# Kernel optimization log

Measured on AMD Instinct MI355X. Metric: run time of the kernel, lower is better.

## Reference

```python
import jax, jax.numpy as jnp
import numpy as np

B = 8
T_SCALES = 2
SEQ_LEN = 720
PRED_LEN = 720
ENC_IN = 862
MARK = 4
D_MODEL = 256
N_HEADS = 8
D_FF = 512
D_BLOCK = 720  # == PRED_LEN -> align is Identity
E_LAYERS = 2
EPS = 1e-5


def _ln(x, g, b):
    m = x.mean(-1, keepdims=True)
    v = ((x - m) ** 2).mean(-1, keepdims=True)
    return (x - m) / jnp.sqrt(v + EPS) * g + b


def setup_inputs() -> dict:
    key = jax.random.key(0)
    ks = iter(jax.random.split(key, 64))
    def rn(shape, s=0.02):
        return jax.random.normal(next(ks), shape, jnp.float32) * s
    L, d = E_LAYERS, D_MODEL
    inp = {}
    inp["multi_batch_x"] = jax.random.normal(next(ks), (B, T_SCALES, SEQ_LEN, ENC_IN), jnp.float32)
    inp["multi_batch_x_mark"] = jax.random.normal(next(ks), (B, T_SCALES, SEQ_LEN, MARK), jnp.float32)
    inp["x_dec"] = jnp.zeros((1,), jnp.float32)
    inp["x_mark_dec"] = jnp.zeros((1,), jnp.float32)
    inp["embed_w"] = rn((d, SEQ_LEN)); inp["embed_b"] = jnp.zeros((d,), jnp.float32)
    for nm in ("Wq", "Wk", "Wv", "Wo", "W3", "W4"):
        inp[nm] = rn((L, d, d))
    for nm in ("bq", "bk", "bv", "bo", "b3", "b4"):
        inp[nm] = jnp.zeros((L, d), jnp.float32)
    inp["W1"] = rn((L, D_FF, d)); inp["b1"] = jnp.zeros((L, D_FF), jnp.float32)
    inp["W2"] = rn((L, d, D_FF)); inp["b2"] = jnp.zeros((L, d), jnp.float32)
    inp["W5"] = rn((L, D_BLOCK, 2 * d)); inp["b5"] = jnp.zeros((L, D_BLOCK), jnp.float32)
    inp["W6"] = rn((L, D_BLOCK, 2 * d)); inp["b6"] = jnp.zeros((L, D_BLOCK), jnp.float32)
    inp["ln1_g"] = jnp.ones((L, d), jnp.float32); inp["ln1_b"] = jnp.zeros((L, d), jnp.float32)
    inp["ln2_g"] = jnp.ones((L, d), jnp.float32); inp["ln2_b"] = jnp.zeros((L, d), jnp.float32)
    return inp


def reference(multi_batch_x, multi_batch_x_mark, x_dec, x_mark_dec,
              embed_w, embed_b, Wq, bq, Wk, bk, Wv, bv, Wo, bo,
              W1, b1, W2, b2, W3, b3, W4, b4, W5, b5, W6, b6,
              ln1_g, ln1_b, ln2_g, ln2_b):
    H = N_HEADS
    E = D_MODEL // H
    Bc = multi_batch_x.shape[0]
    scale = 1.0 / jnp.sqrt(jnp.asarray(E, jnp.float32))
    outs = []
    for t in range(T_SCALES):
        x = multi_batch_x[:, t].transpose(0, 2, 1)            # [B, ENC_IN, S]
        mean = x.mean(-1, keepdims=True)
        std = jnp.sqrt(((x - mean) ** 2).mean(-1, keepdims=True) + EPS)
        xn = (x - mean) / std
        xm = multi_batch_x_mark[:, t].transpose(0, 2, 1)      # [B, MARK, S]
        xin = jnp.concatenate([xn, xm], axis=1)               # [B, N, S], N = ENC_IN+MARK
        h = jnp.einsum('bns,ds->bnd', xin, embed_w) + embed_b  # [B, N, d_model]
        N = xin.shape[1]
        output = jnp.zeros((Bc, N, D_BLOCK), h.dtype)
        for l in range(E_LAYERS):
            # full attention (mask_flag=False), dropout in eval mode = identity
            q = (h @ Wq[l].T + bq[l]).reshape(Bc, N, H, E)
            k = (h @ Wk[l].T + bk[l]).reshape(Bc, N, H, E)
            v = (h @ Wv[l].T + bv[l]).reshape(Bc, N, H, E)
            scores = jnp.einsum('blhe,bshe->bhls', q, k) * scale
            A = jax.nn.softmax(scores, axis=-1)
            att = jnp.einsum('bhls,bshd->blhd', A, v).reshape(Bc, N, H * E)
            x_att = att @ Wo[l].T + bo[l]
            x_ln = _ln(h - x_att, ln1_g[l], ln1_b[l])
            # 1x1 conv FFN (conv over channel dim == linear over feature dim)
            y = jax.nn.gelu(x_ln @ W1[l].T + b1[l], approximate=False) @ W2[l].T + b2[l]
            xs = x_ln - y                                      # subtract-residual
            hh = jax.nn.sigmoid(xs @ W3[l].T + b3[l]) * (xs @ W4[l].T + b4[l])
            cat = jnp.concatenate([x_att, y], axis=-1)         # [B, N, 2*d_model]
            out = jax.nn.sigmoid(cat @ W5[l].T + b5[l]) * (cat @ W6[l].T + b6[l])
            h = _ln(hh, ln2_g[l], ln2_b[l])
            output = out - output
        # align = Identity (D_BLOCK == PRED_LEN); keep first ENC_IN channels, invert scaler
        dec = output[:, :ENC_IN, :] * std + mean               # [B, ENC_IN, PRED_LEN]
        outs.append(dec.transpose(0, 2, 1))                    # [B, PRED_LEN, ENC_IN]
    return jnp.stack(outs, axis=-1).mean(axis=-1)
```

## Files before the change

### kernel.cpp

```cpp
#include <hip/hip_runtime.h>
#include <cstdint>
#include <cstddef>

#define DEV __device__ __forceinline__
#define AS1 __attribute__((address_space(1)))
#define AS3 __attribute__((address_space(3)))

typedef unsigned short u16;
typedef unsigned char u8;
typedef long long ll;

typedef __attribute__((ext_vector_type(8))) __bf16 bf16x8;
typedef __attribute__((ext_vector_type(8))) unsigned short u16x8;
typedef __attribute__((ext_vector_type(4))) float f32x4;

static constexpr int SEQ  = 720;
static constexpr int ENC  = 862;
static constexpr int NTOK = 866;
static constexpr int DM   = 256;
static constexpr int G16  = 16;
static constexpr int MTOT = G16 * NTOK;
static constexpr int KPAD = 768;
static constexpr int SPAD = 896;
static constexpr int TCH  = 15;
static constexpr float SC2 = 0.17677669529663689f * 1.4426950408889634f;

DEV float b2f(u16 v){ union { unsigned u; float f; } x; x.u = ((unsigned)v) << 16; return x.f; }
DEV u16 f2b(float f){ union { float f; unsigned u; } x; x.f = f;
  unsigned r = x.u + 0x7fffu + ((x.u >> 16) & 1u); return (u16)(r >> 16); }
DEV bf16x8 as_bf(u16x8 v){ return __builtin_bit_cast(bf16x8, v); }

DEV void g2l(const u16* g, u16* l){
  __builtin_amdgcn_global_load_lds((AS1 void*)g, (AS3 void*)l, 16, 0, 0);
}

DEV int xcd_work(){
  int L = blockIdx.y * gridDim.x + blockIdx.x;
  int T = gridDim.x * gridDim.y;
  int x = L & 7, k = L >> 3;
  int q = T >> 3, r = T & 7;
  int mn = x < r ? x : r;
  return x*q + mn + k;
}

struct CvtJobs {
  const float* src[10];
  u16* dst[10];
  int n[10];
  int per[10];
  ll stride[10];
};
__global__ __launch_bounds__(256) void cvt_multi(CvtJobs J)
{
  int j = blockIdx.y;
  const float* s = J.src[j];
  u16* d = J.dst[j];
  int n = J.n[j], per = J.per[j];
  ll st = J.stride[j];
  for (int i = blockIdx.x*256 + threadIdx.x; i < n; i += gridDim.x*256) {
    ll di = per ? ((ll)(i/per)*st + (i%per)) : (ll)i;
    d[di] = f2b(s[i]);
  }
}

__global__ __launch_bounds__(256) void pack_bqkv(const float* __restrict__ bq,
                                                 const float* __restrict__ bk,
                                                 const float* __restrict__ bv,
                                                 float* __restrict__ out)
{
  int idx = blockIdx.x*256 + threadIdx.x;
  if (idx >= 1536) return;
  int l = idx / 768, j = idx % 768;
  float v;
  if (j < 256)      v = bq[l*256 + j];
  else if (j < 512) v = bk[l*256 + j - 256];
  else              v = bv[l*256 + j - 512];
  out[idx] = v;
}

__global__ __launch_bounds__(256) void stats_part(const float* __restrict__ x,
                                                  float2* __restrict__ part)
{
  int g  = blockIdx.z;
  int tc = blockIdx.y;
  int c  = (blockIdx.x << 8) + threadIdx.x;
  float s = 0.f, q = 0.f;
  if (c < ENC) {
    const float* xp = x + ((ll)g * SEQ + tc * 48) * ENC + c;
    #pragma unroll 8
    for (int t = 0; t < 48; ++t) {
      float v = xp[(ll)t * ENC];
      s += v; q += v * v;
    }
  }
  part[(((ll)g * TCH + tc) * 4 + blockIdx.x) * 256 + threadIdx.x] = make_float2(s, q);
}

__global__ __launch_bounds__(256) void stats_reduce(const float2* __restrict__ part,
                                                    float* __restrict__ meanp,
                                                    float* __restrict__ stdp)
{
  int g  = blockIdx.x >> 2;
  int cc = blockIdx.x & 3;
  int c  = (cc << 8) + threadIdx.x;
  if (c >= ENC) return;
  float s = 0.f, q = 0.f;
  #pragma unroll
  for (int t = 0; t < TCH; ++t) {
    float2 p = part[(((ll)g * TCH + t) * 4 + cc) * 256 + threadIdx.x];
    s += p.x; q += p.y;
  }
  float mn  = s * (1.f / SEQ);
  float var = q * (1.f / SEQ) - mn * mn;
  var = var < 0.f ? 0.f : var;
  meanp[g * ENC + c] = mn;
  stdp [g * ENC + c] = sqrtf(var + 1e-5f);
}

__global__ __launch_bounds__(256) void build_xin(const float* __restrict__ x,
                                                 const float* __restrict__ xm,
                                                 const float* __restrict__ meanp,
                                                 const float* __restrict__ stdp,
                                                 u16* __restrict__ xin)
{
  int g  = blockIdx.z;
  int c0 = blockIdx.x << 5, s0 = blockIdx.y << 5;
  __shared__ float tl[32][33];
  __shared__ float mn[32], isd[32];
  int tid = threadIdx.x;
  if (tid < 32) {
    int c = c0 + tid;
    float m = 0.f, s = 1.f;
    if (c < ENC) { m = meanp[g*ENC + c]; s = stdp[g*ENC + c]; }
    mn[tid] = m; isd[tid] = 1.f / s;
  }
  __syncthreads();
  int ci = tid & 31, r = tid >> 5;
  #pragma unroll
  for (int p = 0; p < 4; ++p) {
    int sl = r + (p << 3);
    int s = s0 + sl, c = c0 + ci;
    float v = 0.f;
    if (s < SEQ && c < NTOK) {
      if (c < ENC) v = (x[((ll)g*SEQ + s)*ENC + c] - mn[ci]) * isd[ci];
      else         v = xm[((ll)g*SEQ + s)*4 + (c - ENC)];
    }
    tl[sl][ci] = v;
  }
  __syncthreads();
  int si = tid & 31;
  #pragma unroll
  for (int p = 0; p < 4; ++p) {
    int cl = r + (p << 3);
    int c = c0 + cl;
    if (c < NTOK) xin[((ll)g*NTOK + c)*KPAD + s0 + si] = f2b(tl[si][cl]);
  }
}

__global__ __launch_bounds__(256) void pack_embedw(const float* __restrict__ ew,
                                                   u16* __restrict__ wp)
{
  int row = blockIdx.x;
  for (int c = threadIdx.x; c < KPAD; c += 256)
    wp[row*KPAD + c] = (c < SEQ) ? f2b(ew[row*SEQ + c]) : (u16)0;
}

__global__ __launch_bounds__(256) void transpose_v(const u16* __restrict__ v, int ldv,
                                                   u16* __restrict__ vT)
{
  int g = blockIdx.z;
  int d0 = blockIdx.x << 5, s0 = blockIdx.y << 5;
  __shared__ u16 tl[32][33];
  int tid = threadIdx.x;
  int di = tid & 31, r = tid >> 5;
  #pragma unroll
  for (int p = 0; p < 4; ++p) {
    int sl = r + (p << 3);
    int s = s0 + sl;
    u16 val = 0;
    if (s < NTOK) val = v[((ll)g*NTOK + s)*ldv + d0 + di];
    tl[sl][di] = val;
  }
  __syncthreads();
  int si = tid & 31;
  #pragma unroll
  for (int p = 0; p < 4; ++p) {
    int dl = r + (p << 3);
    vT[((ll)g*DM + d0 + dl)*SPAD + s0 + si] = tl[si][dl];
  }
}

__global__ __launch_bounds__(256) void flash_attn(const u16* __restrict__ qb,
                                                  const u16* __restrict__ kb,
                                                  int ldqk,
                                                  const u16* __restrict__ vT,
                                                  u16* __restrict__ attb)
{
  const int w = xcd_work();
  const int gh = w / 7;
  const int g = gh >> 3, h = gh & 7;
  const int q0 = (w % 7) * 128;
  const int tid = threadIdx.x, wv = tid >> 6, lane = tid & 63;
  const int q4 = lane >> 4, c16 = lane & 15;
  constexpr int PLD = 136;

  __shared__ __attribute__((aligned(16))) u16 Qs[128*32];
  __shared__ __attribute__((aligned(16))) u16 Ks[128*32];
  __shared__ __attribute__((aligned(16))) u16 Vs[32*PLD];
  __shared__ __attribute__((aligned(16))) u16 Ps[4][32*PLD];

  {
    int r = tid >> 1, sg = (tid & 1) << 4;
    int row = q0 + r; if (row > NTOK-1) row = NTOK-1;
    const u16* src = qb + ((ll)(g*NTOK + row))*ldqk + h*32 + sg;
    *(uint4*)&Qs[r*32 + sg]     = *(const uint4*)src;
    *(uint4*)&Qs[r*32 + sg + 8] = *(const uint4*)(src + 8);
  }
  __syncthreads();

  bf16x8 qf[2];
  qf[0] = as_bf(*(const u16x8*)&Qs[(wv*32 +      c16)*32 + q4*8]);
  qf[1] = as_bf(*(const u16x8*)&Qs[(wv*32 + 16 + c16)*32 + q4*8]);

  float lsum[2][4] = {{0,0,0,0},{0,0,0,0}};
  f32x4 oacc[2][2];
  oacc[0][0] = (f32x4){0,0,0,0}; oacc[0][1] = (f32x4){0,0,0,0};
  oacc[1][0] = (f32x4){0,0,0,0}; oacc[1][1] = (f32x4){0,0,0,0};

  for (int kt = 0; kt < 7; ++kt) {
    const int k0 = kt * 128;
    if (kt) __syncthreads();
    {
      int r = tid >> 1, sg = (tid & 1) << 4;
      int row = k0 + r; if (row > NTOK-1) row = NTOK-1;
      const u16* src = kb + ((ll)(g*NTOK + row))*ldqk + h*32 + sg;
      *(uint4*)&Ks[r*32 + sg]     = *(const uint4*)src;
      *(uint4*)&Ks[r*32 + sg + 8] = *(const uint4*)(src + 8);
    }
    {
      int e = tid >> 3, sg = (tid & 7) << 4;
      const u16* src = vT + ((ll)(g*DM + h*32 + e))*SPAD + k0 + sg;
      *(uint4*)&Vs[e*PLD + sg]     = *(const uint4*)src;
      *(uint4*)&Vs[e*PLD + sg + 8] = *(const uint4*)(src + 8);
    }
    __syncthreads();

    f32x4 s[2][8];
    #pragma unroll
    for (int i = 0; i < 2; ++i)
      #pragma unroll
      for (int j = 0; j < 8; ++j) s[i][j] = (f32x4){0,0,0,0};
    #pragma unroll
    for (int j = 0; j < 8; ++j) {
      bf16x8 kf = as_bf(*(const u16x8*)&Ks[(j*16 + c16)*32 + q4*8]);
      s[0][j] = __builtin_amdgcn_mfma_f32_16x16x32_bf16(qf[0], kf, s[0][j], 0, 0, 0);
      s[1][j] = __builtin_amdgcn_mfma_f32_16x16x32_bf16(qf[1], kf, s[1][j], 0, 0, 0);
    }
    if (kt == 6) {
      #pragma unroll
      for (int j = 0; j < 8; ++j) {
        if (k0 + j*16 + c16 >= NTOK) {
          #pragma unroll
          for (int r = 0; r < 4; ++r) { s[0][j][r] = -1e30f; s[1][j][r] = -1e30f; }
        }
      }
    }

    #pragma unroll
    for (int i = 0; i < 2; ++i)
      #pragma unroll
      for (int j = 0; j < 8; ++j)
        #pragma unroll
        for (int r = 0; r < 4; ++r) {
          float p = exp2f(s[i][j][r]);
          lsum[i][r] += p;
          unsigned u = __builtin_bit_cast(unsigned, p);
          Ps[wv][(i*16 + q4*4 + r)*PLD + j*16 + c16] = (u16)(u >> 16);
        }

    #pragma unroll
    for (int kk = 0; kk < 4; ++kk) {
      bf16x8 af0 = as_bf(*(const u16x8*)&Ps[wv][(     c16)*PLD + kk*32 + q4*8]);
      bf16x8 af1 = as_bf(*(const u16x8*)&Ps[wv][(16 + c16)*PLD + kk*32 + q4*8]);
      bf16x8 b0  = as_bf(*(const u16x8*)&Vs[(     c16)*PLD + kk*32 + q4*8]);
      bf16x8 b1  = as_bf(*(const u16x8*)&Vs[(16 + c16)*PLD + kk*32 + q4*8]);
      oacc[0][0] = __builtin_amdgcn_mfma_f32_16x16x32_bf16(af0, b0, oacc[0][0], 0, 0, 0);
      oacc[0][1] = __builtin_amdgcn_mfma_f32_16x16x32_bf16(af0, b1, oacc[0][1], 0, 0, 0);
      oacc[1][0] = __builtin_amdgcn_mfma_f32_16x16x32_bf16(af1, b0, oacc[1][0], 0, 0, 0);
      oacc[1][1] = __builtin_amdgcn_mfma_f32_16x16x32_bf16(af1, b1, oacc[1][1], 0, 0, 0);
    }
  }

  float linv[2][4];
  #pragma unroll
  for (int i = 0; i < 2; ++i)
    #pragma unroll
    for (int r = 0; r < 4; ++r) {
      float t = lsum[i][r];
      t += __shfl_xor(t, 1, 64);
      t += __shfl_xor(t, 2, 64);
      t += __shfl_xor(t, 4, 64);
      t += __shfl_xor(t, 8, 64);
      linv[i][r] = 1.f / t;
    }
  #pragma unroll
  for (int i = 0; i < 2; ++i)
    #pragma unroll
    for (int jn = 0; jn < 2; ++jn)
      #pragma unroll
      for (int r = 0; r < 4; ++r) {
        int row = q0 + wv*32 + i*16 + q4*4 + r;
        if (row < NTOK)
          attb[((ll)(g*NTOK + row))*DM + h*32 + jn*16 + c16] =
            f2b(oacc[i][jn][r] * linv[i][r]);
      }
}

__global__ __launch_bounds__(256) void ln_rows(const u16* __restrict__ in1,
                                               const u16* __restrict__ in2,
                                               int ld1, int ld2,
                                               const float* __restrict__ gamma,
                                               const float* __restrict__ beta,
                                               u16* __restrict__ out, int ldo, int Mrows)
{
  int row = blockIdx.x*4 + (threadIdx.x >> 6);
  int lane = threadIdx.x & 63;
  if (row >= Mrows) return;
  float xv[4];
  ushort4 a = *(const ushort4*)(in1 + (ll)row*ld1 + lane*4);
  xv[0]=b2f(a.x); xv[1]=b2f(a.y); xv[2]=b2f(a.z); xv[3]=b2f(a.w);
  if (in2) {
    ushort4 b = *(const ushort4*)(in2 + (ll)row*ld2 + lane*4);
    xv[0]-=b2f(b.x); xv[1]-=b2f(b.y); xv[2]-=b2f(b.z); xv[3]-=b2f(b.w);
  }
  float s = xv[0]+xv[1]+xv[2]+xv[3];
  #pragma unroll
  for (int o = 32; o > 0; o >>= 1) s += __shfl_xor(s, o, 64);
  float mean = s * (1.f/256.f);
  float d0=xv[0]-mean, d1=xv[1]-mean, d2=xv[2]-mean, d3=xv[3]-mean;
  float q = d0*d0 + d1*d1 + d2*d2 + d3*d3;
  #pragma unroll
  for (int o = 32; o > 0; o >>= 1) q += __shfl_xor(q, o, 64);
  float rstd = 1.f / sqrtf(q * (1.f/256.f) + 1e-5f);
  float4 gv = *(const float4*)(gamma + lane*4);
  float4 bb = *(const float4*)(beta  + lane*4);
  ushort4 o4;
  o4.x = f2b(d0*rstd*gv.x + bb.x);
  o4.y = f2b(d1*rstd*gv.y + bb.y);
  o4.z = f2b(d2*rstd*gv.z + bb.z);
  o4.w = f2b(d3*rstd*gv.w + bb.w);
  *(ushort4*)(out + (ll)row*ldo + lane*4) = o4;
}

__global__ __launch_bounds__(256) void final_combine(const u16* __restrict__ outF,
                                                     const float* __restrict__ meanp,
                                                     const float* __restrict__ stdp,
                                                     float* __restrict__ dout)
{
  int b = blockIdx.z;
  int c0 = blockIdx.x << 5, s0 = blockIdx.y << 5;
  __shared__ float tl[32][33];
  int tid = threadIdx.x;
  int si = tid & 31, r = tid >> 5;
  #pragma unroll
  for (int p = 0; p < 4; ++p) {
    int cl = r + (p << 3);
    int c = c0 + cl, s = s0 + si;
    float accv = 0.f;
    #pragma unroll
    for (int t = 0; t < 2; ++t) {
      int g = b*2 + t;
      if (c < ENC && s < SEQ) {
        float v = b2f(outF[((ll)(g*NTOK + c))*SEQ + s]);
        accv += 0.5f * (v * stdp[g*ENC + c] + meanp[g*ENC + c]);
      }
    }
    tl[cl][si] = accv;
  }
  __syncthreads();
  int ci = tid & 31;
  #pragma unroll
  for (int p = 0; p < 4; ++p) {
    int sl = r + (p << 3);
    int s = s0 + sl, c = c0 + ci;
    if (s < SEQ && c < ENC)
      dout[((ll)b*SEQ + s)*ENC + c] = tl[ci][sl];
  }
}

template<int NB>
__global__ __launch_bounds__(256, NB == 1 ? 5 : 3) void gemm64(
    const u16* __restrict__ A, const u16* __restrict__ B0, const u16* __restrict__ B1,
    const float* __restrict__ bias0, const float* __restrict__ bias1,
    u16* __restrict__ C,
    const u16* __restrict__ aux1, u16* __restrict__ aux2, const u16* __restrict__ sub,
    int M, int N, int K, int lda, int ldb, int ldc, int ld1, int ld2, int ldsub, int mode)
{
  __shared__ __attribute__((aligned(16))) u16 S[8192 * (1 + NB)];

  const int tid  = threadIdx.x;
  const int wv   = tid >> 6;
  const int lane = tid & 63;
  const int q4   = lane >> 4;
  const int c16  = lane & 15;

  const int w  = xcd_work();
  const int n0 = (w % gridDim.x) * 64;
  const int m0 = (w / gridDim.x) * 64;
  const int wm = (wv >> 1) * 32;
  const int wn = (wv & 1) * 32;

  const int lrow = lane >> 2;
  const int lcol = (lane & 3) << 3;
  int arow = m0 + wv*16 + lrow; if (arow >= M) arow = M-1;
  int brow = n0 + wv*16 + lrow; if (brow >= N) brow = N-1;
  const u16* pa  = A  + (ll)arow*lda + lcol;
  const u16* pb0 = B0 + (ll)brow*ldb + lcol;
  const u16* pb1 = (NB == 2) ? B1 + (ll)brow*ldb + lcol : nullptr;

  f32x4 acc0[2][2];
  f32x4 acc1[2][2];
  #pragma unroll
  for (int i = 0; i < 2; ++i)
    #pragma unroll
    for (int j = 0; j < 2; ++j) {
      acc0[i][j] = (f32x4){0,0,0,0};
      if constexpr (NB == 2) acc1[i][j] = (f32x4){0,0,0,0};
    }

  const int nk = K >> 6;
  auto issue = [&](int kt2, int p) {
    const int ko = kt2 * 64;
    #pragma unroll
    for (int c = 0; c < 2; ++c) {
      g2l(pa  + ko + c*32, &S[(p*2 + c)*2048 + (wv*16)*32]);
      g2l(pb0 + ko + c*32, &S[8192 + (p*2 + c)*2048 + (wv*16)*32]);
      if constexpr (NB == 2)
        g2l(pb1 + ko + c*32, &S[16384 + (p*2 + c)*2048 + (wv*16)*32]);
    }
  };

  issue(0, 0);
  for (int kt = 0; kt < nk; ++kt) {
    const int p = kt & 1;
    if (kt + 1 < nk) {
      issue(kt + 1, p ^ 1);
      if constexpr (NB == 1) asm volatile("s_waitcnt vmcnt(4)" ::: "memory");
      else                   asm volatile("s_waitcnt vmcnt(6)" ::: "memory");
    } else {
      asm volatile("s_waitcnt vmcnt(0)" ::: "memory");
    }
    __builtin_amdgcn_s_barrier();
    asm volatile("" ::: "memory");

    #pragma unroll
    for (int c = 0; c < 2; ++c) {
      const u16* as_ = &S[(p*2 + c)*2048];
      const u16* bs_ = &S[8192 + (p*2 + c)*2048];
      bf16x8 af[2], bfv[2];
      #pragma unroll
      for (int i = 0; i < 2; ++i)
        af[i] = as_bf(*(const u16x8*)&as_[(wm + i*16 + c16)*32 + q4*8]);
      #pragma unroll
      for (int j = 0; j < 2; ++j)
        bfv[j] = as_bf(*(const u16x8*)&bs_[(wn + j*16 + c16)*32 + q4*8]);
      #pragma unroll
      for (int i = 0; i < 2; ++i)
        #pragma unroll
        for (int j = 0; j < 2; ++j)
          acc0[i][j] = __builtin_amdgcn_mfma_f32_16x16x32_bf16(af[i], bfv[j], acc0[i][j], 0, 0, 0);
      if constexpr (NB == 2) {
        const u16* b2_ = &S[16384 + (p*2 + c)*2048];
        bf16x8 b1v[2];
        #pragma unroll
        for (int j = 0; j < 2; ++j)
          b1v[j] = as_bf(*(const u16x8*)&b2_[(wn + j*16 + c16)*32 + q4*8]);
        #pragma unroll
        for (int i = 0; i < 2; ++i)
          #pragma unroll
          for (int j = 0; j < 2; ++j)
            acc1[i][j] = __builtin_amdgcn_mfma_f32_16x16x32_bf16(af[i], b1v[j], acc1[i][j], 0, 0, 0);
      }
    }

    asm volatile("s_waitcnt lgkmcnt(0)" ::: "memory");
    __builtin_amdgcn_s_barrier();
  }

  #pragma unroll
  for (int i = 0; i < 2; ++i) {
    #pragma unroll
    for (int j = 0; j < 2; ++j) {
      int n = n0 + wn + j*16 + c16;
      if (n >= N) continue;
      float bv0 = bias0 ? bias0[n] : 0.f;
      float bv1 = (NB == 2) ? bias1[n] : 0.f;
      int mb = m0 + wm + i*16 + q4*4;
      #pragma unroll
      for (int r = 0; r < 4; ++r) {
        int m = mb + r;
        if (m >= M) continue;
        ll ci = (ll)m*ldc + n;
        if constexpr (NB == 2) {
          float z5 = acc0[i][j][r] + bv0;
          float z6 = acc1[i][j][r] + bv1;
          float v = z6 / (1.f + expf(-z5));
          if (sub) v -= b2f(sub[(ll)m*ldsub + n]);
          C[ci] = f2b(v);
        } else {
          float x = acc0[i][j][r] + bv0;
          if (mode == 0) {
            C[ci] = f2b(x);
          } else if (mode == 1) {
            C[ci] = f2b(0.5f * x * (1.f + erff(x * 0.70710678118654752f)));
          } else if (mode == 5) {
            C[ci] = f2b(n < 256 ? x * SC2 : x);
          } else {
            C[ci] = f2b(x);
            float xl = b2f(aux1[(ll)m*ld1 + n]);
            aux2[(ll)m*ld2 + n] = f2b(xl - x);
          }
        }
      }
    }
  }
}

extern "C" void kernel_launch(void* const* d_in, const int* in_sizes, int n_in,
                              void* d_out, int out_size, void* d_ws, size_t ws_size,
                              hipStream_t stream)
{
  (void)in_sizes; (void)n_in; (void)out_size; (void)ws_size;
  const float* x    = (const float*)d_in[0];
  const float* xm   = (const float*)d_in[1];
  const float* embw = (const float*)d_in[4];
  const float* embb = (const float*)d_in[5];
  const float* Wqf  = (const float*)d_in[6];
  const float* Wkf  = (const float*)d_in[7];
  const float* Wvf  = (const float*)d_in[8];
  const float* Wof  = (const float*)d_in[9];
  const float* W3f  = (const float*)d_in[10];
  const float* W4f  = (const float*)d_in[11];
  const float* bq   = (const float*)d_in[12];
  const float* bk   = (const float*)d_in[13];
  const float* bv   = (const float*)d_in[14];
  const float* bo   = (const float*)d_in[15];
  const float* b3   = (const float*)d_in[16];
  const float* b4   = (const float*)d_in[17];
  const float* W1f  = (const float*)d_in[18];
  const float* b1   = (const float*)d_in[19];
  const float* W2f  = (const float*)d_in[20];
  const float* b2   = (const float*)d_in[21];
  const float* W5f  = (const float*)d_in[22];
  const float* b5   = (const float*)d_in[23];
  const float* W6f  = (const float*)d_in[24];
  const float* b6   = (const float*)d_in[25];
  const float* ln1g = (const float*)d_in[26];
  const float* ln1b = (const float*)d_in[27];
  const float* ln2g = (const float*)d_in[28];
  const float* ln2b = (const float*)d_in[29];

  u8* ws = (u8*)d_ws;
  size_t off = 0;
  auto alloc = [&](size_t bytes) -> void* {
    void* ptr = ws + off;
    off = (off + bytes + 255) & ~(size_t)255;
    return ptr;
  };
  float* meanp = (float*)alloc((size_t)G16*ENC*4);
  float* stdp  = (float*)alloc((size_t)G16*ENC*4);
  float* partp = (float*)alloc((size_t)G16*TCH*1024*2*4);
  u16* xin   = (u16*)alloc((size_t)G16*NTOK*KPAD*2);
  u16* wp    = (u16*)alloc((size_t)DM*KPAD*2);
  const int nWsm = 2*DM*DM;
  const int nWff = 2*512*DM;
  const int nW56 = 2*SEQ*512;
  u16* Wqkv = (u16*)alloc((size_t)2*768*256*2);
  u16* Wo = (u16*)alloc((size_t)nWsm*2);
  u16* W3 = (u16*)alloc((size_t)nWsm*2);
  u16* W4 = (u16*)alloc((size_t)nWsm*2);
  u16* W1 = (u16*)alloc((size_t)nWff*2);
  u16* W2 = (u16*)alloc((size_t)nWff*2);
  u16* W5 = (u16*)alloc((size_t)nW56*2);
  u16* W6 = (u16*)alloc((size_t)nW56*2);
  float* bqkv = (float*)alloc((size_t)2*768*4);
  u16* hb    = (u16*)alloc((size_t)MTOT*DM*2);
  u16* qkvb  = (u16*)alloc((size_t)MTOT*768*2);
  u16* vT    = (u16*)alloc((size_t)G16*DM*SPAD*2);
  u16* attb  = (u16*)alloc((size_t)MTOT*DM*2);
  u16* catb  = (u16*)alloc((size_t)MTOT*512*2);
  u16* xlnb  = (u16*)alloc((size_t)MTOT*DM*2);
  u16* t1b   = (u16*)alloc((size_t)MTOT*512*2);
  u16* xsb   = (u16*)alloc((size_t)MTOT*DM*2);
  u16* hhb   = (u16*)alloc((size_t)MTOT*DM*2);
  u16* out0b = (u16*)alloc((size_t)MTOT*SEQ*2);
  u16* outFb = (u16*)alloc((size_t)MTOT*SEQ*2);

  auto gemm64_1 = [&](const u16* A, int lda, const u16* B, int ldb, const float* bias,
                      u16* C, int ldc, int M, int N, int K, int mode,
                      const u16* a1, int ld1, u16* a2, int ld2) {
    dim3 grid((N + 63) / 64, (M + 63) / 64, 1);
    gemm64<1><<<grid, 256, 0, stream>>>(A, B, nullptr, bias, nullptr, C, a1, a2, nullptr,
                                        M, N, K, lda, ldb, ldc, ld1, ld2, 0, mode);
  };
  auto gemm64_2 = [&](const u16* A, int lda, const u16* B0p, const u16* B1p, int ldb,
                      const float* bias0, const float* bias1, u16* C, int ldc,
                      const u16* sub, int ldsub, int M, int N, int K) {
    dim3 grid((N + 63) / 64, (M + 63) / 64, 1);
    gemm64<2><<<grid, 256, 0, stream>>>(A, B0p, B1p, bias0, bias1, C, nullptr, nullptr, sub,
                                        M, N, K, lda, ldb, ldc, 0, 0, ldsub, 0);
  };

  CvtJobs J{};
  int nj = 0;
  auto addjob = [&](const float* s, u16* d, int n, int per, ll stride) {
    J.src[nj] = s; J.dst[nj] = d; J.n[nj] = n; J.per[nj] = per; J.stride[nj] = stride; nj++;
  };
  addjob(Wqf, Wqkv,           nWsm, 65536, 196608);
  addjob(Wkf, Wqkv + 65536,   nWsm, 65536, 196608);
  addjob(Wvf, Wqkv + 131072,  nWsm, 65536, 196608);
  addjob(Wof, Wo, nWsm, 0, 0);
  addjob(W3f, W3, nWsm, 0, 0);
  addjob(W4f, W4, nWsm, 0, 0);
  addjob(W1f, W1, nWff, 0, 0);
  addjob(W2f, W2, nWff, 0, 0);
  addjob(W5f, W5, nW56, 0, 0);
  addjob(W6f, W6, nW56, 0, 0);
  cvt_multi<<<dim3(512, 10), 256, 0, stream>>>(J);
  pack_bqkv<<<6, 256, 0, stream>>>(bq, bk, bv, bqkv);

  stats_part<<<dim3(4, TCH, 16), 256, 0, stream>>>(x, (float2*)partp);
  stats_reduce<<<64, 256, 0, stream>>>((const float2*)partp, meanp, stdp);
  build_xin<<<dim3(28, 24, 16), 256, 0, stream>>>(x, xm, meanp, stdp, xin);
  pack_embedw<<<256, 256, 0, stream>>>(embw, wp);

  gemm64_1(xin, KPAD, wp, KPAD, embb, hb, DM, MTOT, DM, KPAD, 0, nullptr, 0, nullptr, 0);

  for (int l = 0; l < 2; ++l) {
    const ll wOff = (ll)l * DM * DM;
    gemm64_1(hb, DM, Wqkv + (ll)l*768*256, 256, bqkv + l*768, qkvb, 768,
             MTOT, 768, DM, 5, nullptr, 0, nullptr, 0);
    transpose_v<<<dim3(8, 28, 16), 256, 0, stream>>>(qkvb + 512, 768, vT);

    flash_attn<<<dim3(7, 128), 256, 0, stream>>>(qkvb, qkvb + 256, 768, vT, attb);

    gemm64_1(attb, DM, Wo + wOff, DM, bo + l*DM, catb, 512, MTOT, DM, DM, 0, nullptr, 0, nullptr, 0);
    ln_rows<<<MTOT/4, 256, 0, stream>>>(hb, catb, DM, 512, ln1g + l*DM, ln1b + l*DM, xlnb, DM, MTOT);
    gemm64_1(xlnb, DM, W1 + (ll)l*512*DM, DM, b1 + l*512, t1b, 512, MTOT, 512, DM, 1, nullptr, 0, nullptr, 0);
    gemm64_1(t1b, 512, W2 + (ll)l*DM*512, 512, b2 + l*DM, catb + 256, 512, MTOT, DM, 512, 2, xlnb, DM, xsb, DM);
    gemm64_2(xsb, DM, W3 + wOff, W4 + wOff, DM, b3 + l*DM, b4 + l*DM, hhb, DM,
             nullptr, 0, MTOT, DM, DM);
    ln_rows<<<MTOT/4, 256, 0, stream>>>(hhb, nullptr, DM, 0, ln2g + l*DM, ln2b + l*DM, hb, DM, MTOT);
    if (l == 0)
      gemm64_2(catb, 512, W5 + (ll)l*SEQ*512, W6 + (ll)l*SEQ*512, 512,
               b5 + l*SEQ, b6 + l*SEQ, out0b, SEQ, nullptr, 0, MTOT, SEQ, 512);
    else
      gemm64_2(catb, 512, W5 + (ll)l*SEQ*512, W6 + (ll)l*SEQ*512, 512,
               b5 + l*SEQ, b6 + l*SEQ, outFb, SEQ, out0b, SEQ, MTOT, SEQ, 512);
  }

  final_combine<<<dim3(27, 23, 8), 256, 0, stream>>>(outFb, meanp, stdp, (float*)d_out);
}
```

Measured before the change: 611.7 us.

## Enlarge dual-B GEMM M-tile to 128 and XOR-swizzle LDS layout

The dual-weight gated GEMM (W5/W6 path) now computes 128-row M tiles instead of 64, so each staged B0/B1 tile is reused across twice as many A rows and fewer blocks re-read the weights. It also XOR-swizzles the 16-byte column chunks in shared memory for both loads and fragment reads, in both GEMM variants, to reduce LDS bank conflicts. In exchange the dual kernel uses more LDS and registers, its occupancy hint drops from 3 to 2 blocks, and the grid is halved along M, which could leave compute units underused.

```diff
diff --git a/kernel.cpp b/kernel.cpp
--- a/kernel.cpp
+++ b/kernel.cpp
@@ -389,14 +389,20 @@
 }
 
 template<int NB>
-__global__ __launch_bounds__(256, NB == 1 ? 5 : 3) void gemm64(
+__global__ __launch_bounds__(256, NB == 1 ? 5 : 2) void gemm64(
     const u16* __restrict__ A, const u16* __restrict__ B0, const u16* __restrict__ B1,
     const float* __restrict__ bias0, const float* __restrict__ bias1,
     u16* __restrict__ C,
     const u16* __restrict__ aux1, u16* __restrict__ aux2, const u16* __restrict__ sub,
     int M, int N, int K, int lda, int ldb, int ldc, int ld1, int ld2, int ldsub, int mode)
 {
-  __shared__ __attribute__((aligned(16))) u16 S[8192 * (1 + NB)];
+  constexpr int BM  = (NB == 2) ? 128 : 64;
+  constexpr int MI  = (NB == 2) ? 4 : 2;
+  constexpr int APC = BM * 32;
+  constexpr int B0O = 4 * APC;
+  constexpr int B1O = B0O + 8192;
+  constexpr int SSZ = (NB == 2) ? 32768 : 16384;
+  __shared__ __attribute__((aligned(16))) u16 S[SSZ];
 
   const int tid  = threadIdx.x;
   const int wv   = tid >> 6;
@@ -406,22 +412,29 @@
 
   const int w  = xcd_work();
   const int n0 = (w % gridDim.x) * 64;
-  const int m0 = (w / gridDim.x) * 64;
-  const int wm = (wv >> 1) * 32;
+  const int m0 = (w / gridDim.x) * BM;
+  const int wm = (wv >> 1) * (BM / 2);
   const int wn = (wv & 1) * 32;
 
   const int lrow = lane >> 2;
-  const int lcol = (lane & 3) << 3;
-  int arow = m0 + wv*16 + lrow; if (arow >= M) arow = M-1;
-  int brow = n0 + wv*16 + lrow; if (brow >= N) brow = N-1;
-  const u16* pa  = A  + (ll)arow*lda + lcol;
-  const u16* pb0 = B0 + (ll)brow*ldb + lcol;
-  const u16* pb1 = (NB == 2) ? B1 + (ll)brow*ldb + lcol : nullptr;
-
-  f32x4 acc0[2][2];
-  f32x4 acc1[2][2];
-  #pragma unroll
-  for (int i = 0; i < 2; ++i)
+  const int lcol = (((lane & 3) ^ ((lrow >> 1) & 3)) << 3);
+
+  int br = n0 + wv*16 + lrow; if (br >= N) br = N - 1;
+  const u16* pb0 = B0 + (ll)br*ldb + lcol;
+  const u16* pb1 = (NB == 2) ? B1 + (ll)br*ldb + lcol : nullptr;
+
+  int ar0, ar1 = 0;
+  if constexpr (NB == 2) { ar0 = m0 + wv*32 + lrow; ar1 = ar0 + 16; }
+  else                   { ar0 = m0 + wv*16 + lrow; }
+  if (ar0 >= M) ar0 = M - 1;
+  if (NB == 2 && ar1 >= M) ar1 = M - 1;
+  const u16* pa0 = A + (ll)ar0*lda + lcol;
+  const u16* pa1 = (NB == 2) ? A + (ll)ar1*lda + lcol : nullptr;
+
+  f32x4 acc0[MI][2];
+  f32x4 acc1[MI][2];
+  #pragma unroll
+  for (int i = 0; i < MI; ++i)
     #pragma unroll
     for (int j = 0; j < 2; ++j) {
       acc0[i][j] = (f32x4){0,0,0,0};
@@ -433,10 +446,15 @@
     const int ko = kt2 * 64;
     #pragma unroll
     for (int c = 0; c < 2; ++c) {
-      g2l(pa  + ko + c*32, &S[(p*2 + c)*2048 + (wv*16)*32]);
-      g2l(pb0 + ko + c*32, &S[8192 + (p*2 + c)*2048 + (wv*16)*32]);
+      if constexpr (NB == 2) {
+        g2l(pa0 + ko + c*32, &S[(p*2 + c)*APC + (wv*32)*32]);
+        g2l(pa1 + ko + c*32, &S[(p*2 + c)*APC + (wv*32 + 16)*32]);
+      } else {
+        g2l(pa0 + ko + c*32, &S[(p*2 + c)*APC + (wv*16)*32]);
+      }
+      g2l(pb0 + ko + c*32, &S[B0O + (p*2 + c)*2048 + (wv*16)*32]);
       if constexpr (NB == 2)
-        g2l(pb1 + ko + c*32, &S[16384 + (p*2 + c)*2048 + (wv*16)*32]);
+        g2l(pb1 + ko + c*32, &S[B1O + (p*2 + c)*2048 + (wv*16)*32]);
     }
   };
 
@@ -446,37 +464,38 @@
     if (kt + 1 < nk) {
       issue(kt + 1, p ^ 1);
       if constexpr (NB == 1) asm volatile("s_waitcnt vmcnt(4)" ::: "memory");
-      else                   asm volatile("s_waitcnt vmcnt(6)" ::: "memory");
+      else                   asm volatile("s_waitcnt vmcnt(8)" ::: "memory");
     } else {
       asm volatile("s_waitcnt vmcnt(0)" ::: "memory");
     }
     __builtin_amdgcn_s_barrier();
     asm volatile("" ::: "memory");
 
+    const int sw = ((q4 ^ ((c16 >> 1) & 3)) << 3);
     #pragma unroll
     for (int c = 0; c < 2; ++c) {
-      const u16* as_ = &S[(p*2 + c)*2048];
-      const u16* bs_ = &S[8192 + (p*2 + c)*2048];
-      bf16x8 af[2], bfv[2];
-      #pragma unroll
-      for (int i = 0; i < 2; ++i)
-        af[i] = as_bf(*(const u16x8*)&as_[(wm + i*16 + c16)*32 + q4*8]);
+      const u16* as_ = &S[(p*2 + c)*APC];
+      const u16* b0s = &S[B0O + (p*2 + c)*2048];
+      bf16x8 af[MI], bfv[2];
+      #pragma unroll
+      for (int i = 0; i < MI; ++i)
+        af[i] = as_bf(*(const u16x8*)&as_[(wm + i*16 + c16)*32 + sw]);
       #pragma unroll
       for (int j = 0; j < 2; ++j)
-        bfv[j] = as_bf(*(const u16x8*)&bs_[(wn + j*16 + c16)*32 + q4*8]);
-      #pragma unroll
-      for (int i = 0; i < 2; ++i)
+        bfv[j] = as_bf(*(const u16x8*)&b0s[(wn + j*16 + c16)*32 + sw]);
+      #pragma unroll
+      for (int i = 0; i < MI; ++i)
         #pragma unroll
         for (int j = 0; j < 2; ++j)
           acc0[i][j] = __builtin_amdgcn_mfma_f32_16x16x32_bf16(af[i], bfv[j], acc0[i][j], 0, 0, 0);
       if constexpr (NB == 2) {
-        const u16* b2_ = &S[16384 + (p*2 + c)*2048];
+        const u16* b1s = &S[B1O + (p*2 + c)*2048];
         bf16x8 b1v[2];
         #pragma unroll
         for (int j = 0; j < 2; ++j)
-          b1v[j] = as_bf(*(const u16x8*)&b2_[(wn + j*16 + c16)*32 + q4*8]);
+          b1v[j] = as_bf(*(const u16x8*)&b1s[(wn + j*16 + c16)*32 + sw]);
         #pragma unroll
-        for (int i = 0; i < 2; ++i)
+        for (int i = 0; i < MI; ++i)
           #pragma unroll
           for (int j = 0; j < 2; ++j)
             acc1[i][j] = __builtin_amdgcn_mfma_f32_16x16x32_bf16(af[i], b1v[j], acc1[i][j], 0, 0, 0);
@@ -488,7 +507,7 @@
   }
 
   #pragma unroll
-  for (int i = 0; i < 2; ++i) {
+  for (int i = 0; i < MI; ++i) {
     #pragma unroll
     for (int j = 0; j < 2; ++j) {
       int n = n0 + wn + j*16 + c16;
@@ -606,7 +625,7 @@
   auto gemm64_2 = [&](const u16* A, int lda, const u16* B0p, const u16* B1p, int ldb,
                       const float* bias0, const float* bias1, u16* C, int ldc,
                       const u16* sub, int ldsub, int M, int N, int K) {
-    dim3 grid((N + 63) / 64, (M + 63) / 64, 1);
+    dim3 grid((N + 63) / 64, (M + 127) / 128, 1);
     gemm64<2><<<grid, 256, 0, stream>>>(A, B0p, B1p, bias0, bias1, C, nullptr, nullptr, sub,
                                         M, N, K, lda, ldb, ldc, 0, 0, ldsub, 0);
   };
```

New measurement: 623.9 us. No clear change (+2.0%).
